# Optimization experiments

Hardware: AMD Instinct MI355X
Metric: run time of the kernel (lower is better)

Reference implementation:

```python
import jax, jax.numpy as jnp
import numpy as np

N = 20000      # nodes
E = 320000     # edges
IN = 128       # in_channels
HID = 64       # hidden_channels (per-head out dim, concat=False -> mean over heads)
HEADS = 4
NEG_SLOPE = 0.2


def setup_inputs() -> dict:
    key = jax.random.key(0)
    ks = jax.random.split(key, 18)
    g = lambda i, shape: jax.random.normal(ks[i], shape, dtype=jnp.float32) * 0.05
    return {
        "x": jax.random.normal(ks[0], (N, IN), dtype=jnp.float32),
        "edge_index": jax.random.randint(ks[1], (2, E), 0, N),
        # GATConv params: lin weight (no bias in PyG lin), att_src/att_dst, out bias
        "W0": g(2, (IN, HEADS * HID)),
        "W1": g(3, (HID, HEADS * HID)),
        "W2": g(4, (HID, HEADS * HID)),
        "W3": g(5, (HID, HEADS * HID)),
        "a_src": g(6, (4, HEADS, HID)),
        "a_dst": g(7, (4, HEADS, HID)),
        "gat_b": g(8, (4, HID)),
        # residual projection for layer 0 (in_channels != hidden_channels)
        "res_W": g(9, (IN, HID)),
        "res_b": g(10, (HID,)),
        # edge classifier MLP: 2*HID -> HID -> HID -> 1
        "lin_W0": g(11, (2 * HID, HID)),
        "lin_b0": g(12, (HID,)),
        "lin_W1": g(13, (HID, HID)),
        "lin_b1": g(14, (HID,)),
        "lin_W2": g(15, (HID, 1)),
        "lin_b2": g(16, (1,)),
    }


def gat_conv(x, src, dst, W, asrc, adst, b, n):
    # x: [n, F_in]; src/dst: [E_tot] (self-loops included); W: [F_in, H*C]
    h = (x @ W).reshape(n, HEADS, HID)                     # [n, H, C]
    s_src = (h * asrc).sum(-1)                             # [n, H]
    s_dst = (h * adst).sum(-1)                             # [n, H]
    e = jax.nn.leaky_relu(s_src[src] + s_dst[dst], NEG_SLOPE)  # [E_tot, H]
    # segment softmax over incoming edges of each dst node
    m = jax.ops.segment_max(e, dst, num_segments=n)        # [n, H]
    p = jnp.exp(e - m[dst])
    z = jax.ops.segment_sum(p, dst, num_segments=n)
    alpha = p / z[dst]                                     # [E_tot, H]
    out = jax.ops.segment_sum(alpha[:, :, None] * h[src], dst, num_segments=n)  # [n, H, C]
    return out.mean(axis=1) + b                            # concat=False -> mean over heads


def reference(x, edge_index, W0, W1, W2, W3, a_src, a_dst, gat_b,
              res_W, res_b, lin_W0, lin_b0, lin_W1, lin_b1, lin_W2, lin_b2):
    n = x.shape[0]
    loop = jnp.arange(n)
    src = jnp.concatenate([edge_index[0], loop])  # PyG GATConv adds self-loops
    dst = jnp.concatenate([edge_index[1], loop])
    Ws = [W0, W1, W2, W3]
    h = x
    for i in range(4):
        h_prev = h
        h = gat_conv(h, src, dst, Ws[i], a_src[i], a_dst[i], gat_b[i], n)
        if i == 0:
            h = h + h_prev @ res_W + res_b   # projected residual
        else:
            h = h + h_prev
        h = jax.nn.elu(h)
    row, col = edge_index[0], edge_index[1]
    er = jnp.concatenate([h[row], h[col]], axis=1)        # [E, 2*HID]
    er = jax.nn.relu(er @ lin_W0 + lin_b0)                # shapes differ -> no residual
    er = jax.nn.relu(er @ lin_W1 + lin_b1 + er)           # shapes match -> residual
    logits = er @ lin_W2 + lin_b2                          # [E, 1]
    return logits
```

## Files before the change

kernel.cpp:

```cpp
#include <hip/hip_runtime.h>
#include <hip/hip_bf16.h>

#define NSLOPE 0.2f

typedef short bf16x8 __attribute__((ext_vector_type(8)));
typedef float f32x4 __attribute__((ext_vector_type(4)));

__device__ __forceinline__ unsigned short f2b(float f) {
    unsigned u = __float_as_uint(f);
    unsigned r = (u + 0x7FFFu + ((u >> 16) & 1u)) >> 16;
    return (unsigned short)r;
}
__device__ __forceinline__ float b2f_lo(unsigned w) {
    return __uint_as_float(w << 16);
}
__device__ __forceinline__ float b2f_hi(unsigned w) {
    return __uint_as_float(w & 0xFFFF0000u);
}
__device__ __forceinline__ float b2f_s(short s) {
    return __uint_as_float(((unsigned)(unsigned short)s) << 16);
}
__device__ __forceinline__ unsigned packb(float lo, float hi) {
    return ((unsigned)f2b(hi) << 16) | (unsigned)f2b(lo);
}


__global__ __launch_bounds__(256) void hist_deg(const int* __restrict__ ei,
                                                int* __restrict__ deg, int E,
                                                int n) {
    int t = blockIdx.x * 256 + threadIdx.x;
    int Etot = E + n;
    if (t >= Etot) return;
    int d = (t < E) ? ei[E + t] : (t - E);
    atomicAdd(&deg[d], 1);
}

__global__ __launch_bounds__(256) void scan_blk(const int* __restrict__ deg,
                                                int* __restrict__ local,
                                                int* __restrict__ bsum, int n) {
    __shared__ int sm[256];
    const int base = blockIdx.x * 1024;
    const int t = threadIdx.x;
    const int i0 = base + t * 4;
    int v0 = 0, v1 = 0, v2 = 0, v3 = 0;
    if (i0 + 3 < n) {
        int4 v = *(const int4*)(deg + i0);
        v0 = v.x; v1 = v.y; v2 = v.z; v3 = v.w;
    } else {
        if (i0 < n) v0 = deg[i0];
        if (i0 + 1 < n) v1 = deg[i0 + 1];
        if (i0 + 2 < n) v2 = deg[i0 + 2];
    }
    int s = v0 + v1 + v2 + v3;
    sm[t] = s;
    __syncthreads();
    for (int off = 1; off < 256; off <<= 1) {
        int val = (t >= off) ? sm[t - off] : 0;
        __syncthreads();
        sm[t] += val;
        __syncthreads();
    }
    int ex = sm[t] - s;
    if (t == 255) bsum[blockIdx.x] = sm[255];
    if (i0 < n) local[i0] = ex;
    if (i0 + 1 < n) local[i0 + 1] = ex + v0;
    if (i0 + 2 < n) local[i0 + 2] = ex + v0 + v1;
    if (i0 + 3 < n) local[i0 + 3] = ex + v0 + v1 + v2;
}

__global__ __launch_bounds__(256) void scan_top(const int* __restrict__ bsum,
                                                int* __restrict__ boff,
                                                int nb) {
    __shared__ int sm[256];
    const int t = threadIdx.x;
    int s = (t < nb) ? bsum[t] : 0;
    sm[t] = s;
    __syncthreads();
    for (int off = 1; off < 256; off <<= 1) {
        int val = (t >= off) ? sm[t - off] : 0;
        __syncthreads();
        sm[t] += val;
        __syncthreads();
    }
    if (t < nb) boff[t] = sm[t] - s;
}

__global__ __launch_bounds__(256) void scan_add(const int* __restrict__ local,
                                                const int* __restrict__ boff,
                                                int* __restrict__ rowstart,
                                                int* __restrict__ cursor,
                                                int n, int Etot) {
    int i = blockIdx.x * 256 + threadIdx.x;
    if (i > n) return;
    if (i == n) {
        rowstart[n] = Etot;
        return;
    }
    int v = local[i] + boff[i >> 10];
    rowstart[i] = v;
    cursor[i] = v;
}

__global__ __launch_bounds__(256) void fill_csr(const int* __restrict__ ei,
                                                int* __restrict__ cursor,
                                                int2* __restrict__ csr2, int E,
                                                int n) {
    int t = blockIdx.x * 256 + threadIdx.x;
    int Etot = E + n;
    if (t >= Etot) return;
    int s, d;
    if (t < E) { s = ei[t]; d = ei[E + t]; } else { s = d = t - E; }
    int pos = atomicAdd(&cursor[d], 1);
    csr2[pos] = make_int2(s, d);
}

__global__ __launch_bounds__(256) void prep_weights(
    const float* __restrict__ W0, const float* __restrict__ W1,
    const float* __restrict__ W2, const float* __restrict__ W3,
    const float* __restrict__ resW, const float* __restrict__ linW0,
    const float* __restrict__ linW1, const float* __restrict__ linB0,
    short* __restrict__ WtC0, short* __restrict__ WtC1,
    short* __restrict__ WtC2, short* __restrict__ WtC3,
    short* __restrict__ WtR, short* __restrict__ WtU, short* __restrict__ WtV,
    short* __restrict__ WbT, float* __restrict__ bias128) {
    const int bx = blockIdx.x;
    if (bx < 4) {
        const float* src = (bx == 0) ? W0 : (bx == 1) ? W1 : (bx == 2) ? W2 : W3;
        short* dst = (bx == 0) ? WtC0 : (bx == 1) ? WtC1 : (bx == 2) ? WtC2 : WtC3;
        const int K = (bx == 0) ? 128 : 64;
        const int total = 64 * 4 * K;
        for (int idx = blockIdx.y * 256 + threadIdx.x; idx < total;
             idx += 256 * 16) {
            int j = idx / (4 * K);
            int rem = idx - j * 4 * K;
            int h = rem / K, k = rem - h * K;
            dst[idx] = (short)f2b(src[k * 256 + h * 64 + j]);
        }
        return;
    }
    const float* src;
    short* dst;
    int K, NC, rowoff = 0;
    switch (bx) {
        case 4: src = resW; dst = WtR; K = 128; NC = 64; break;
        case 5: src = linW0; dst = WtU; K = 64; NC = 64; break;
        case 6: src = linW0; dst = WtV; K = 64; NC = 64; rowoff = 64; break;
        case 7: src = linW1; dst = WbT; K = 64; NC = 64; break;
        default: {
            if (blockIdx.y == 0 && threadIdx.x < 128)
                bias128[threadIdx.x] =
                    (threadIdx.x < 64) ? linB0[threadIdx.x] : 0.f;
            return;
        }
    }
    for (int idx = blockIdx.y * 256 + threadIdx.x; idx < K * NC;
         idx += 256 * 16) {
        int k = idx / NC, nn = idx - k * NC;
        dst[nn * K + k] = (short)f2b(src[(k + rowoff) * NC + nn]);
    }
}

__global__ __launch_bounds__(256) void prep_wsd(
    const float* __restrict__ W0, const float* __restrict__ W1,
    const float* __restrict__ W2, const float* __restrict__ W3,
    const float* __restrict__ a_src, const float* __restrict__ a_dst,
    float* __restrict__ wsd0, float* __restrict__ wsdL) {
    const int l = blockIdx.x;
    const float* W = (l == 0) ? W0 : (l == 1) ? W1 : (l == 2) ? W2 : W3;
    const int K = (l == 0) ? 128 : 64;
    float* dst = (l == 0) ? wsd0 : wsdL + (l - 1) * 64 * 8;
    for (int idx = threadIdx.x; idx < K * 8; idx += 256) {
        int k = idx >> 3, j = idx & 7, h = j & 3;
        const float* av = ((j < 4) ? a_src : a_dst) + l * 256 + h * 64;
        const float* wr = W + k * 256 + h * 64;
        float s = 0.f;
#pragma unroll 8
        for (int c = 0; c < 64; ++c) s += wr[c] * av[c];
        dst[k * 8 + j] = s;
    }
}

__global__ __launch_bounds__(256) void convert_x_scores(
    const float* __restrict__ x, const float* __restrict__ wsd0,
    unsigned* __restrict__ xb2, float* __restrict__ Ssrc,
    float* __restrict__ Sdst, int n) {
    const int wid = threadIdx.x >> 6;
    const int lane = threadIdx.x & 63;
    const int node = blockIdx.x * 4 + wid;
    if (node >= n) return;
    float2 xv = *(const float2*)&x[(size_t)node * 128 + lane * 2];
    xb2[(size_t)node * 64 + lane] = packb(xv.x, xv.y);
    float pv[8];
    const float* w0 = &wsd0[(lane * 2) * 8];
    const float* w1 = &wsd0[(lane * 2 + 1) * 8];
#pragma unroll
    for (int j = 0; j < 8; ++j) pv[j] = xv.x * w0[j] + xv.y * w1[j];
#pragma unroll
    for (int off = 1; off < 64; off <<= 1) {
#pragma unroll
        for (int j = 0; j < 8; ++j) pv[j] += __shfl_xor(pv[j], off, 64);
    }
    if (lane == 0) {
        *(float4*)&Ssrc[node * 4] = make_float4(pv[0], pv[1], pv[2], pv[3]);
        *(float4*)&Sdst[node * 4] = make_float4(pv[4], pv[5], pv[6], pv[7]);
    }
}

template <int K, int NG, int OM>
__global__ __launch_bounds__(256) void mfma_gemm(
    const short* __restrict__ Xb, const short* __restrict__ Wt,
    const float* __restrict__ bias, float* __restrict__ OutF,
    short* __restrict__ OutB, int n) {
    constexpr int XSTR = K + 8;
    constexpr int NC = NG * 16;
    __shared__ __align__(16) short Xs[64 * XSTR];
    __shared__ __align__(16) short Ws[NC * 40];
    const int tid = threadIdx.x;
    const int nb = blockIdx.x * 64;
    constexpr int CH = K / 8;
    for (int idx = tid; idx < 64 * CH; idx += 256) {
        int row = idx / CH, c = idx - row * CH;
        uint4 v = make_uint4(0, 0, 0, 0);
        if (nb + row < n)
            v = *(const uint4*)(Xb + (size_t)(nb + row) * K + c * 8);
        *(uint4*)(Xs + row * XSTR + c * 8) = v;
    }
    const int wid = tid >> 6;
    const int lane = tid & 63;
    const int t = lane & 15, quad = lane >> 4;
    f32x4 acc[NG];
#pragma unroll
    for (int g = 0; g < NG; ++g) acc[g] = (f32x4){0.f, 0.f, 0.f, 0.f};
#pragma unroll 1
    for (int kc = 0; kc < K / 32; ++kc) {
        __syncthreads();
        for (int idx = tid; idx < NC * 4; idx += 256) {
            int row = idx >> 2, c = idx & 3;
            uint4 v = *(const uint4*)(Wt + (size_t)row * K + kc * 32 + c * 8);
            *(uint4*)(Ws + row * 40 + c * 8) = v;
        }
        __syncthreads();
        bf16x8 a =
            *(const bf16x8*)(Xs + (wid * 16 + t) * XSTR + kc * 32 + quad * 8);
#pragma unroll
        for (int g = 0; g < NG; ++g) {
            bf16x8 b = *(const bf16x8*)(Ws + (g * 16 + t) * 40 + quad * 8);
            acc[g] = __builtin_amdgcn_mfma_f32_16x16x32_bf16(a, b, acc[g], 0, 0, 0);
        }
    }
    float bv[NG];
#pragma unroll
    for (int g = 0; g < NG; ++g) bv[g] = bias ? bias[g * 16 + t] : 0.f;
#pragma unroll
    for (int r = 0; r < 4; ++r) {
        int node = nb + wid * 16 + quad * 4 + r;
        if (node >= n) continue;
        if (OM == 0) {
#pragma unroll
            for (int g = 0; g < NG; ++g)
                OutF[(size_t)node * NC + g * 16 + t] = acc[g][r] + bv[g];
        } else {
#pragma unroll
            for (int g = 0; g < NG; ++g)
                OutB[(size_t)node * NC + g * 16 + t] =
                    (short)f2b(acc[g][r] + bv[g]);
        }
    }
}

template <int KK, bool SCORES>
__global__ __launch_bounds__(256) void gemm_layer(
    const short* __restrict__ Xb, const short* __restrict__ Wt,
    const float* __restrict__ gbias, const float* __restrict__ resid,
    const float* __restrict__ wsd, float* __restrict__ feat,
    short* __restrict__ featb, float* __restrict__ Ssrc,
    float* __restrict__ Sdst, int n) {
    __shared__ __align__(16) short Xs[64 * 136];
    __shared__ __align__(16) short Ws[64 * 40];
    const int tid = threadIdx.x;
    const int nb = blockIdx.x * 64;
    const int wid = tid >> 6;
    const int lane = tid & 63;
    const int t = lane & 15, quad = lane >> 4;
    f32x4 acc[4];
#pragma unroll
    for (int g = 0; g < 4; ++g) acc[g] = (f32x4){0.f, 0.f, 0.f, 0.f};
#pragma unroll 1
    for (int c0 = 0; c0 < KK / 128; ++c0) {
        __syncthreads();
        for (int idx = tid; idx < 1024; idx += 256) {
            int row = idx >> 4, c = idx & 15;
            uint4 v = make_uint4(0, 0, 0, 0);
            if (nb + row < n)
                v = *(const uint4*)(Xb + (size_t)(nb + row) * KK + c0 * 128 +
                                    c * 8);
            *(uint4*)(Xs + row * 136 + c * 8) = v;
        }
#pragma unroll 1
        for (int kc = 0; kc < 4; ++kc) {
            __syncthreads();
            for (int idx = tid; idx < 256; idx += 256) {
                int row = idx >> 2, c = idx & 3;
                uint4 v = *(const uint4*)(Wt + (size_t)row * KK + c0 * 128 +
                                          kc * 32 + c * 8);
                *(uint4*)(Ws + row * 40 + c * 8) = v;
            }
            __syncthreads();
            bf16x8 a =
                *(const bf16x8*)(Xs + (wid * 16 + t) * 136 + kc * 32 + quad * 8);
#pragma unroll
            for (int g = 0; g < 4; ++g) {
                bf16x8 b = *(const bf16x8*)(Ws + (g * 16 + t) * 40 + quad * 8);
                acc[g] =
                    __builtin_amdgcn_mfma_f32_16x16x32_bf16(a, b, acc[g], 0, 0, 0);
            }
        }
    }
    float bv[4];
#pragma unroll
    for (int g = 0; g < 4; ++g) bv[g] = gbias[g * 16 + t];
    float wsv[4][8];
    if (SCORES) {
#pragma unroll
        for (int g = 0; g < 4; ++g) {
            float4 lo = *(const float4*)&wsd[(g * 16 + t) * 8];
            float4 hi = *(const float4*)&wsd[(g * 16 + t) * 8 + 4];
            wsv[g][0] = lo.x; wsv[g][1] = lo.y; wsv[g][2] = lo.z;
            wsv[g][3] = lo.w; wsv[g][4] = hi.x; wsv[g][5] = hi.y;
            wsv[g][6] = hi.z; wsv[g][7] = hi.w;
        }
    }
#pragma unroll
    for (int r = 0; r < 4; ++r) {
        int node = nb + wid * 16 + quad * 4 + r;
        bool ok = node < n;
        float val[4];
#pragma unroll
        for (int g = 0; g < 4; ++g) {
            float v = acc[g][r] + bv[g];
            if (ok) v += resid[(size_t)node * 64 + g * 16 + t];
            v = v > 0.f ? v : expm1f(v);
            val[g] = v;
            if (ok) {
                feat[(size_t)node * 64 + g * 16 + t] = v;
                featb[(size_t)node * 64 + g * 16 + t] = (short)f2b(v);
            }
        }
        if (SCORES) {
            float pv[8];
#pragma unroll
            for (int j = 0; j < 8; ++j) {
                pv[j] = val[0] * wsv[0][j] + val[1] * wsv[1][j] +
                        val[2] * wsv[2][j] + val[3] * wsv[3][j];
            }
#pragma unroll
            for (int off = 1; off < 16; off <<= 1) {
#pragma unroll
                for (int j = 0; j < 8; ++j) pv[j] += __shfl_xor(pv[j], off, 64);
            }
            if (t == 0 && ok) {
                *(float4*)&Ssrc[node * 4] =
                    make_float4(pv[0], pv[1], pv[2], pv[3]);
                *(float4*)&Sdst[node * 4] =
                    make_float4(pv[4], pv[5], pv[6], pv[7]);
            }
        }
    }
}

__global__ __launch_bounds__(256) void edge_scores(
    const int2* __restrict__ csr2, const float* __restrict__ Ssrc,
    const float* __restrict__ Sdst, float4* __restrict__ p4, int Etot) {
    int e = blockIdx.x * 256 + threadIdx.x;
    if (e >= Etot) return;
    int2 sd = csr2[e];
    float4 ss = *(const float4*)&Ssrc[sd.x * 4];
    float4 dd = *(const float4*)&Sdst[sd.y * 4];
    float c0 = ss.x + dd.x, c1 = ss.y + dd.y, c2 = ss.z + dd.z,
          c3 = ss.w + dd.w;
    c0 = c0 > 0.f ? c0 : NSLOPE * c0;
    c1 = c1 > 0.f ? c1 : NSLOPE * c1;
    c2 = c2 > 0.f ? c2 : NSLOPE * c2;
    c3 = c3 > 0.f ? c3 : NSLOPE * c3;
    p4[e] = make_float4(__expf(c0), __expf(c1), __expf(c2), __expf(c3));
}

__global__ __launch_bounds__(256) void gat_gather128(
    const int2* __restrict__ csr2, const int* __restrict__ rowstart,
    const float4* __restrict__ p4, const unsigned* __restrict__ xin,
    unsigned* __restrict__ aggB, int n) {
    const int wid = threadIdx.x >> 6;
    const int lane = threadIdx.x & 63;
    const int node = blockIdx.x * 4 + wid;
    if (node >= n) return;
    const int start = rowstart[node];
    const int end = rowstart[node + 1];
    float u00 = 0.f, u01 = 0.f, u10 = 0.f, u11 = 0.f;
    float u20 = 0.f, u21 = 0.f, u30 = 0.f, u31 = 0.f;
    float z0 = 0.f, z1 = 0.f, z2 = 0.f, z3 = 0.f;
#pragma unroll 4
    for (int e = start; e < end; ++e) {
        int sj = csr2[e].x;
        float4 p = p4[e];
        unsigned fv = xin[(size_t)sj * 64 + lane];
        float f0 = b2f_lo(fv), f1 = b2f_hi(fv);
        u00 += p.x * f0; u01 += p.x * f1;
        u10 += p.y * f0; u11 += p.y * f1;
        u20 += p.z * f0; u21 += p.z * f1;
        u30 += p.w * f0; u31 += p.w * f1;
        z0 += p.x; z1 += p.y; z2 += p.z; z3 += p.w;
    }
    float i0 = 0.25f / z0, i1 = 0.25f / z1, i2 = 0.25f / z2, i3 = 0.25f / z3;
    size_t base = (size_t)node * 256;
    aggB[base + lane] = packb(u00 * i0, u01 * i0);
    aggB[base + 64 + lane] = packb(u10 * i1, u11 * i1);
    aggB[base + 128 + lane] = packb(u20 * i2, u21 * i2);
    aggB[base + 192 + lane] = packb(u30 * i3, u31 * i3);
}

__global__ __launch_bounds__(256) void gat_gather64(
    const int2* __restrict__ csr2, const int* __restrict__ rowstart,
    const float4* __restrict__ p4, const unsigned* __restrict__ fin,
    unsigned* __restrict__ aggB, int n) {
    const int wid = threadIdx.x >> 6;
    const int lane = threadIdx.x & 63;
    const int half = lane >> 5;
    const int cl = lane & 31;
    const int node = blockIdx.x * 4 + wid;
    if (node >= n) return;
    const int start = rowstart[node];
    const int end = rowstart[node + 1];
    float u00 = 0.f, u01 = 0.f, u10 = 0.f, u11 = 0.f;
    float u20 = 0.f, u21 = 0.f, u30 = 0.f, u31 = 0.f;
    float z0 = 0.f, z1 = 0.f, z2 = 0.f, z3 = 0.f;
#pragma unroll 4
    for (int e = start + half; e < end; e += 2) {
        int sj = csr2[e].x;
        float4 p = p4[e];
        unsigned fv = fin[(size_t)sj * 32 + cl];
        float f0 = b2f_lo(fv), f1 = b2f_hi(fv);
        u00 += p.x * f0; u01 += p.x * f1;
        u10 += p.y * f0; u11 += p.y * f1;
        u20 += p.z * f0; u21 += p.z * f1;
        u30 += p.w * f0; u31 += p.w * f1;
        z0 += p.x; z1 += p.y; z2 += p.z; z3 += p.w;
    }
    u00 += __shfl_xor(u00, 32, 64); u01 += __shfl_xor(u01, 32, 64);
    u10 += __shfl_xor(u10, 32, 64); u11 += __shfl_xor(u11, 32, 64);
    u20 += __shfl_xor(u20, 32, 64); u21 += __shfl_xor(u21, 32, 64);
    u30 += __shfl_xor(u30, 32, 64); u31 += __shfl_xor(u31, 32, 64);
    z0 += __shfl_xor(z0, 32, 64); z1 += __shfl_xor(z1, 32, 64);
    z2 += __shfl_xor(z2, 32, 64); z3 += __shfl_xor(z3, 32, 64);
    if (half == 0) {
        float i0 = 0.25f / z0, i1 = 0.25f / z1, i2 = 0.25f / z2,
              i3 = 0.25f / z3;
        size_t base = (size_t)node * 128;
        aggB[base + cl] = packb(u00 * i0, u01 * i0);
        aggB[base + 32 + cl] = packb(u10 * i1, u11 * i1);
        aggB[base + 64 + cl] = packb(u20 * i2, u21 * i2);
        aggB[base + 96 + cl] = packb(u30 * i3, u31 * i3);
    }
}

__global__ __launch_bounds__(256) void edge_mlp3(
    const int* __restrict__ ei, const unsigned* __restrict__ UV,
    const short* __restrict__ WbT, const float* __restrict__ bb,
    const float* __restrict__ Wc, const float* __restrict__ bc,
    float* __restrict__ out, int E) {
    __shared__ __align__(16) short t1b[64 * 72];
    __shared__ __align__(16) short wbs[64 * 72];
    const int tid = threadIdx.x;
    const int eBase = blockIdx.x * 64;
    for (int idx = tid; idx < 512; idx += 256) {
        int row = idx >> 3, c = idx & 7;
        *(uint4*)(wbs + row * 72 + c * 8) =
            *(const uint4*)(WbT + row * 64 + c * 8);
    }
    {
        const int j = tid & 31;
        const int eg = tid >> 5;
        int rr[8], cc[8];
#pragma unroll
        for (int it = 0; it < 8; ++it) {
            int e = eBase + it * 8 + eg;
            rr[it] = (e < E) ? ei[e] : 0;
            cc[it] = (e < E) ? ei[E + e] : 0;
        }
#pragma unroll
        for (int it = 0; it < 8; ++it) {
            unsigned uu = UV[(size_t)rr[it] * 64 + j];
            unsigned vv = UV[(size_t)cc[it] * 64 + 32 + j];
            float lo = fmaxf(b2f_lo(uu) + b2f_lo(vv), 0.f);
            float hi = fmaxf(b2f_hi(uu) + b2f_hi(vv), 0.f);
            *(unsigned*)(t1b + (it * 8 + eg) * 72 + j * 2) = packb(lo, hi);
        }
    }
    __syncthreads();
    const int w = tid >> 6, lane = tid & 63;
    const int t = lane & 15, quad = lane >> 4;
    f32x4 acc[4];
#pragma unroll
    for (int g = 0; g < 4; ++g) acc[g] = (f32x4){0.f, 0.f, 0.f, 0.f};
#pragma unroll
    for (int kc = 0; kc < 2; ++kc) {
        bf16x8 a = *(const bf16x8*)(t1b + (w * 16 + t) * 72 + kc * 32 + quad * 8);
#pragma unroll
        for (int g = 0; g < 4; ++g) {
            bf16x8 b = *(const bf16x8*)(wbs + (g * 16 + t) * 72 + kc * 32 + quad * 8);
            acc[g] = __builtin_amdgcn_mfma_f32_16x16x32_bf16(a, b, acc[g], 0, 0, 0);
        }
    }
    float wcv[4], bbv[4];
#pragma unroll
    for (int g = 0; g < 4; ++g) {
        wcv[g] = Wc[g * 16 + t];
        bbv[g] = bb[g * 16 + t];
    }
    const float bcv = bc[0];
#pragma unroll
    for (int r = 0; r < 4; ++r) {
        int el = w * 16 + quad * 4 + r;
        float part = 0.f;
#pragma unroll
        for (int g = 0; g < 4; ++g) {
            float t1v = b2f_s(t1b[el * 72 + g * 16 + t]);
            float t2 = fmaxf(acc[g][r] + bbv[g] + t1v, 0.f);
            part += t2 * wcv[g];
        }
        part += __shfl_xor(part, 1, 64);
        part += __shfl_xor(part, 2, 64);
        part += __shfl_xor(part, 4, 64);
        part += __shfl_xor(part, 8, 64);
        int e = eBase + el;
        if (t == 0 && e < E) out[e] = part + bcv;
    }
}

extern "C" void kernel_launch(void* const* d_in, const int* in_sizes, int n_in,
                              void* d_out, int out_size, void* d_ws,
                              size_t ws_size, hipStream_t stream) {
    const float* x = (const float*)d_in[0];
    const int* ei = (const int*)d_in[1];
    const float* W0 = (const float*)d_in[2];
    const float* W1 = (const float*)d_in[3];
    const float* W2 = (const float*)d_in[4];
    const float* W3 = (const float*)d_in[5];
    const float* a_src = (const float*)d_in[6];
    const float* a_dst = (const float*)d_in[7];
    const float* gat_b = (const float*)d_in[8];
    const float* res_W = (const float*)d_in[9];
    const float* res_b = (const float*)d_in[10];
    const float* lin_W0 = (const float*)d_in[11];
    const float* lin_b0 = (const float*)d_in[12];
    const float* lin_W1 = (const float*)d_in[13];
    const float* lin_b1 = (const float*)d_in[14];
    const float* lin_W2 = (const float*)d_in[15];
    const float* lin_b2 = (const float*)d_in[16];
    float* out = (float*)d_out;

    const int N = in_sizes[0] / 128;
    const int E = in_sizes[1] / 2;
    const int Etot = E + N;

    char* ws = (char*)d_ws;
    unsigned* aggB = (unsigned*)ws;
    float* featA = (float*)(aggB + (size_t)N * 256);
    float* featB = featA + (size_t)N * 64;
    short* featbA = (short*)(featB + (size_t)N * 64);
    short* featbB = featbA + (size_t)N * 64;
    float* res = (float*)(featbB + (size_t)N * 64);
    short* xb = (short*)(res + (size_t)N * 64);
    float* Ssrc = (float*)(xb + (size_t)N * 128);
    float* Sdst = Ssrc + (size_t)N * 4;
    short* WtC0 = (short*)(Sdst + (size_t)N * 4);
    short* WtC1 = WtC0 + 64 * 512;
    short* WtC2 = WtC1 + 64 * 256;
    short* WtC3 = WtC2 + 64 * 256;
    short* WtR = WtC3 + 64 * 256;
    short* WtU = WtR + 64 * 128;
    short* WtV = WtU + 64 * 64;
    short* WbT = WtV + 64 * 64;
    float* wsd0 = (float*)(WbT + 64 * 64);
    float* wsdL = wsd0 + 128 * 8;
    float* bias128 = wsdL + 3 * 64 * 8;
    int* deg = (int*)(bias128 + 128);
    int* rowstart = deg + N;
    int* cursor = rowstart + N + 1;
    int* locals = cursor + N;
    int* bsum = locals + N;
    int* boff = bsum + 256;
    int2* csr2 = (int2*)(((size_t)(boff + 256) + 15) & ~(size_t)15);
    float4* p4 = (float4*)(((size_t)(csr2 + Etot) + 15) & ~(size_t)15);
    unsigned* UVb = aggB;

    const int gemmBlocks = (N + 63) / 64;
    const int edgeBlocks = (Etot + 255) / 256;
    const int nodeW = (N + 3) / 4;
    const int scanBlocks = (N + 1023) / 1024;

    hipMemsetAsync(deg, 0, (size_t)N * sizeof(int), stream);
    hist_deg<<<edgeBlocks, 256, 0, stream>>>(ei, deg, E, N);
    scan_blk<<<scanBlocks, 256, 0, stream>>>(deg, locals, bsum, N);
    scan_top<<<1, 256, 0, stream>>>(bsum, boff, scanBlocks);
    scan_add<<<(N + 256) / 256, 256, 0, stream>>>(locals, boff, rowstart,
                                                  cursor, N, Etot);
    fill_csr<<<edgeBlocks, 256, 0, stream>>>(ei, cursor, csr2, E, N);

    prep_weights<<<dim3(9, 16), 256, 0, stream>>>(
        W0, W1, W2, W3, res_W, lin_W0, lin_W1, lin_b0, WtC0, WtC1, WtC2, WtC3,
        WtR, WtU, WtV, WbT, bias128);
    prep_wsd<<<4, 256, 0, stream>>>(W0, W1, W2, W3, a_src, a_dst, wsd0, wsdL);
    convert_x_scores<<<nodeW, 256, 0, stream>>>(x, wsd0, (unsigned*)xb, Ssrc,
                                                Sdst, N);
    mfma_gemm<128, 4, 0><<<gemmBlocks, 256, 0, stream>>>(xb, WtR, res_b, res,
                                                         nullptr, N);

    edge_scores<<<edgeBlocks, 256, 0, stream>>>(csr2, Ssrc, Sdst, p4, Etot);
    gat_gather128<<<nodeW, 256, 0, stream>>>(csr2, rowstart, p4,
                                             (const unsigned*)xb, aggB, N);
    gemm_layer<512, true><<<gemmBlocks, 256, 0, stream>>>(
        (const short*)aggB, WtC0, gat_b, res, wsdL, featA, featbA, Ssrc, Sdst,
        N);
    const short* WtCs[3] = {WtC1, WtC2, WtC3};
    float* feats[4] = {featA, featB, featA, featB};
    short* featbs[4] = {featbA, featbB, featbA, featbB};
    for (int i = 1; i < 4; ++i) {
        edge_scores<<<edgeBlocks, 256, 0, stream>>>(csr2, Ssrc, Sdst, p4, Etot);
        gat_gather64<<<nodeW, 256, 0, stream>>>(
            csr2, rowstart, p4, (const unsigned*)featbs[i - 1], aggB, N);
        if (i < 3)
            gemm_layer<256, true><<<gemmBlocks, 256, 0, stream>>>(
                (const short*)aggB, WtCs[i - 1], gat_b + i * 64, feats[i - 1],
                wsdL + i * 64 * 8, feats[i], featbs[i], Ssrc, Sdst, N);
        else
            gemm_layer<256, false><<<gemmBlocks, 256, 0, stream>>>(
                (const short*)aggB, WtCs[i - 1], gat_b + i * 64, feats[i - 1],
                nullptr, feats[i], featbs[i], Ssrc, Sdst, N);
    }

    mfma_gemm<64, 8, 2><<<gemmBlocks, 256, 0, stream>>>(
        featbB, WtU, bias128, nullptr, (short*)UVb, N);
    edge_mlp3<<<(E + 63) / 64, 256, 0, stream>>>(ei, UVb, WbT, lin_b1, lin_W2,
                                                 lin_b2, out, E);
}
```

Before: 353.7 us.

## Fuse edge score computation into gather kernels and shrink CSR to source-only indices

```diff
diff --git a/kernel.cpp b/kernel.cpp
--- a/kernel.cpp
+++ b/kernel.cpp
@@ -103,7 +103,7 @@
 
 __global__ __launch_bounds__(256) void fill_csr(const int* __restrict__ ei,
                                                 int* __restrict__ cursor,
-                                                int2* __restrict__ csr2, int E,
+                                                int* __restrict__ csrS, int E,
                                                 int n) {
     int t = blockIdx.x * 256 + threadIdx.x;
     int Etot = E + n;
@@ -111,7 +111,7 @@
     int s, d;
     if (t < E) { s = ei[t]; d = ei[E + t]; } else { s = d = t - E; }
     int pos = atomicAdd(&cursor[d], 1);
-    csr2[pos] = make_int2(s, d);
+    csrS[pos] = s;
 }
 
 __global__ __launch_bounds__(256) void prep_weights(
@@ -368,49 +368,61 @@
     }
 }
 
-__global__ __launch_bounds__(256) void edge_scores(
-    const int2* __restrict__ csr2, const float* __restrict__ Ssrc,
-    const float* __restrict__ Sdst, float4* __restrict__ p4, int Etot) {
-    int e = blockIdx.x * 256 + threadIdx.x;
-    if (e >= Etot) return;
-    int2 sd = csr2[e];
-    float4 ss = *(const float4*)&Ssrc[sd.x * 4];
-    float4 dd = *(const float4*)&Sdst[sd.y * 4];
-    float c0 = ss.x + dd.x, c1 = ss.y + dd.y, c2 = ss.z + dd.z,
-          c3 = ss.w + dd.w;
-    c0 = c0 > 0.f ? c0 : NSLOPE * c0;
-    c1 = c1 > 0.f ? c1 : NSLOPE * c1;
-    c2 = c2 > 0.f ? c2 : NSLOPE * c2;
-    c3 = c3 > 0.f ? c3 : NSLOPE * c3;
-    p4[e] = make_float4(__expf(c0), __expf(c1), __expf(c2), __expf(c3));
-}
-
 __global__ __launch_bounds__(256) void gat_gather128(
-    const int2* __restrict__ csr2, const int* __restrict__ rowstart,
-    const float4* __restrict__ p4, const unsigned* __restrict__ xin,
-    unsigned* __restrict__ aggB, int n) {
+    const int* __restrict__ csrS, const int* __restrict__ rowstart,
+    const float* __restrict__ Ssrc, const float* __restrict__ Sdst,
+    const unsigned* __restrict__ xin, unsigned* __restrict__ aggB, int n) {
     const int wid = threadIdx.x >> 6;
     const int lane = threadIdx.x & 63;
     const int node = blockIdx.x * 4 + wid;
     if (node >= n) return;
     const int start = rowstart[node];
     const int end = rowstart[node + 1];
+    const float4 sd = *(const float4*)&Sdst[node * 4];
     float u00 = 0.f, u01 = 0.f, u10 = 0.f, u11 = 0.f;
     float u20 = 0.f, u21 = 0.f, u30 = 0.f, u31 = 0.f;
-    float z0 = 0.f, z1 = 0.f, z2 = 0.f, z3 = 0.f;
+    float zp0 = 0.f, zp1 = 0.f, zp2 = 0.f, zp3 = 0.f;
+    for (int base = start; base < end; base += 64) {
+        const int cnt = min(64, end - base);
+        int sreg = 0;
+        float p0r = 0.f, p1r = 0.f, p2r = 0.f, p3r = 0.f;
+        if (lane < cnt) {
+            sreg = csrS[base + lane];
+            float4 ss = *(const float4*)&Ssrc[sreg * 4];
+            float c0 = ss.x + sd.x, c1 = ss.y + sd.y;
+            float c2 = ss.z + sd.z, c3 = ss.w + sd.w;
+            c0 = c0 > 0.f ? c0 : NSLOPE * c0;
+            c1 = c1 > 0.f ? c1 : NSLOPE * c1;
+            c2 = c2 > 0.f ? c2 : NSLOPE * c2;
+            c3 = c3 > 0.f ? c3 : NSLOPE * c3;
+            p0r = __expf(c0); p1r = __expf(c1);
+            p2r = __expf(c2); p3r = __expf(c3);
+            zp0 += p0r; zp1 += p1r; zp2 += p2r; zp3 += p3r;
+        }
 #pragma unroll 4
-    for (int e = start; e < end; ++e) {
-        int sj = csr2[e].x;
-        float4 p = p4[e];
-        unsigned fv = xin[(size_t)sj * 64 + lane];
-        float f0 = b2f_lo(fv), f1 = b2f_hi(fv);
-        u00 += p.x * f0; u01 += p.x * f1;
-        u10 += p.y * f0; u11 += p.y * f1;
-        u20 += p.z * f0; u21 += p.z * f1;
-        u30 += p.w * f0; u31 += p.w * f1;
-        z0 += p.x; z1 += p.y; z2 += p.z; z3 += p.w;
-    }
-    float i0 = 0.25f / z0, i1 = 0.25f / z1, i2 = 0.25f / z2, i3 = 0.25f / z3;
+        for (int j = 0; j < cnt; ++j) {
+            int sj = __shfl(sreg, j, 64);
+            float p0 = __shfl(p0r, j, 64);
+            float p1 = __shfl(p1r, j, 64);
+            float p2 = __shfl(p2r, j, 64);
+            float p3 = __shfl(p3r, j, 64);
+            unsigned fv = xin[(size_t)sj * 64 + lane];
+            float f0 = b2f_lo(fv), f1 = b2f_hi(fv);
+            u00 += p0 * f0; u01 += p0 * f1;
+            u10 += p1 * f0; u11 += p1 * f1;
+            u20 += p2 * f0; u21 += p2 * f1;
+            u30 += p3 * f0; u31 += p3 * f1;
+        }
+    }
+#pragma unroll
+    for (int off = 1; off < 64; off <<= 1) {
+        zp0 += __shfl_xor(zp0, off, 64);
+        zp1 += __shfl_xor(zp1, off, 64);
+        zp2 += __shfl_xor(zp2, off, 64);
+        zp3 += __shfl_xor(zp3, off, 64);
+    }
+    float i0 = 0.25f / zp0, i1 = 0.25f / zp1;
+    float i2 = 0.25f / zp2, i3 = 0.25f / zp3;
     size_t base = (size_t)node * 256;
     aggB[base + lane] = packb(u00 * i0, u01 * i0);
     aggB[base + 64 + lane] = packb(u10 * i1, u11 * i1);
@@ -419,9 +431,9 @@
 }
 
 __global__ __launch_bounds__(256) void gat_gather64(
-    const int2* __restrict__ csr2, const int* __restrict__ rowstart,
-    const float4* __restrict__ p4, const unsigned* __restrict__ fin,
-    unsigned* __restrict__ aggB, int n) {
+    const int* __restrict__ csrS, const int* __restrict__ rowstart,
+    const float* __restrict__ Ssrc, const float* __restrict__ Sdst,
+    const unsigned* __restrict__ fin, unsigned* __restrict__ aggB, int n) {
     const int wid = threadIdx.x >> 6;
     const int lane = threadIdx.x & 63;
     const int half = lane >> 5;
@@ -430,30 +442,59 @@
     if (node >= n) return;
     const int start = rowstart[node];
     const int end = rowstart[node + 1];
+    const float4 sd = *(const float4*)&Sdst[node * 4];
     float u00 = 0.f, u01 = 0.f, u10 = 0.f, u11 = 0.f;
     float u20 = 0.f, u21 = 0.f, u30 = 0.f, u31 = 0.f;
-    float z0 = 0.f, z1 = 0.f, z2 = 0.f, z3 = 0.f;
+    float zp0 = 0.f, zp1 = 0.f, zp2 = 0.f, zp3 = 0.f;
+    for (int base = start; base < end; base += 64) {
+        const int cnt = min(64, end - base);
+        int sreg = 0;
+        float p0r = 0.f, p1r = 0.f, p2r = 0.f, p3r = 0.f;
+        if (lane < cnt) {
+            sreg = csrS[base + lane];
+            float4 ss = *(const float4*)&Ssrc[sreg * 4];
+            float c0 = ss.x + sd.x, c1 = ss.y + sd.y;
+            float c2 = ss.z + sd.z, c3 = ss.w + sd.w;
+            c0 = c0 > 0.f ? c0 : NSLOPE * c0;
+            c1 = c1 > 0.f ? c1 : NSLOPE * c1;
+            c2 = c2 > 0.f ? c2 : NSLOPE * c2;
+            c3 = c3 > 0.f ? c3 : NSLOPE * c3;
+            p0r = __expf(c0); p1r = __expf(c1);
+            p2r = __expf(c2); p3r = __expf(c3);
+            zp0 += p0r; zp1 += p1r; zp2 += p2r; zp3 += p3r;
+        }
 #pragma unroll 4
-    for (int e = start + half; e < end; e += 2) {
-        int sj = csr2[e].x;
-        float4 p = p4[e];
-        unsigned fv = fin[(size_t)sj * 32 + cl];
-        float f0 = b2f_lo(fv), f1 = b2f_hi(fv);
-        u00 += p.x * f0; u01 += p.x * f1;
-        u10 += p.y * f0; u11 += p.y * f1;
-        u20 += p.z * f0; u21 += p.z * f1;
-        u30 += p.w * f0; u31 += p.w * f1;
-        z0 += p.x; z1 += p.y; z2 += p.z; z3 += p.w;
+        for (int j = 0; j < cnt; j += 2) {
+            int idx = j + half;
+            int sj = __shfl(sreg, idx, 64);
+            float p0 = __shfl(p0r, idx, 64);
+            float p1 = __shfl(p1r, idx, 64);
+            float p2 = __shfl(p2r, idx, 64);
+            float p3 = __shfl(p3r, idx, 64);
+            if (idx < cnt) {
+                unsigned fv = fin[(size_t)sj * 32 + cl];
+                float f0 = b2f_lo(fv), f1 = b2f_hi(fv);
+                u00 += p0 * f0; u01 += p0 * f1;
+                u10 += p1 * f0; u11 += p1 * f1;
+                u20 += p2 * f0; u21 += p2 * f1;
+                u30 += p3 * f0; u31 += p3 * f1;
+            }
+        }
     }
     u00 += __shfl_xor(u00, 32, 64); u01 += __shfl_xor(u01, 32, 64);
     u10 += __shfl_xor(u10, 32, 64); u11 += __shfl_xor(u11, 32, 64);
     u20 += __shfl_xor(u20, 32, 64); u21 += __shfl_xor(u21, 32, 64);
     u30 += __shfl_xor(u30, 32, 64); u31 += __shfl_xor(u31, 32, 64);
-    z0 += __shfl_xor(z0, 32, 64); z1 += __shfl_xor(z1, 32, 64);
-    z2 += __shfl_xor(z2, 32, 64); z3 += __shfl_xor(z3, 32, 64);
+#pragma unroll
+    for (int off = 1; off < 64; off <<= 1) {
+        zp0 += __shfl_xor(zp0, off, 64);
+        zp1 += __shfl_xor(zp1, off, 64);
+        zp2 += __shfl_xor(zp2, off, 64);
+        zp3 += __shfl_xor(zp3, off, 64);
+    }
     if (half == 0) {
-        float i0 = 0.25f / z0, i1 = 0.25f / z1, i2 = 0.25f / z2,
-              i3 = 0.25f / z3;
+        float i0 = 0.25f / zp0, i1 = 0.25f / zp1;
+        float i2 = 0.25f / zp2, i3 = 0.25f / zp3;
         size_t base = (size_t)node * 128;
         aggB[base + cl] = packb(u00 * i0, u01 * i0);
         aggB[base + 32 + cl] = packb(u10 * i1, u11 * i1);
@@ -589,8 +630,7 @@
     int* locals = cursor + N;
     int* bsum = locals + N;
     int* boff = bsum + 256;
-    int2* csr2 = (int2*)(((size_t)(boff + 256) + 15) & ~(size_t)15);
-    float4* p4 = (float4*)(((size_t)(csr2 + Etot) + 15) & ~(size_t)15);
+    int* csrS = boff + 256;
     unsigned* UVb = aggB;
 
     const int gemmBlocks = (N + 63) / 64;
@@ -604,7 +644,7 @@
     scan_top<<<1, 256, 0, stream>>>(bsum, boff, scanBlocks);
     scan_add<<<(N + 256) / 256, 256, 0, stream>>>(locals, boff, rowstart,
                                                   cursor, N, Etot);
-    fill_csr<<<edgeBlocks, 256, 0, stream>>>(ei, cursor, csr2, E, N);
+    fill_csr<<<edgeBlocks, 256, 0, stream>>>(ei, cursor, csrS, E, N);
 
     prep_weights<<<dim3(9, 16), 256, 0, stream>>>(
         W0, W1, W2, W3, res_W, lin_W0, lin_W1, lin_b0, WtC0, WtC1, WtC2, WtC3,
@@ -615,8 +655,7 @@
     mfma_gemm<128, 4, 0><<<gemmBlocks, 256, 0, stream>>>(xb, WtR, res_b, res,
                                                          nullptr, N);
 
-    edge_scores<<<edgeBlocks, 256, 0, stream>>>(csr2, Ssrc, Sdst, p4, Etot);
-    gat_gather128<<<nodeW, 256, 0, stream>>>(csr2, rowstart, p4,
+    gat_gather128<<<nodeW, 256, 0, stream>>>(csrS, rowstart, Ssrc, Sdst,
                                              (const unsigned*)xb, aggB, N);
     gemm_layer<512, true><<<gemmBlocks, 256, 0, stream>>>(
         (const short*)aggB, WtC0, gat_b, res, wsdL, featA, featbA, Ssrc, Sdst,
@@ -625,9 +664,9 @@
     float* feats[4] = {featA, featB, featA, featB};
     short* featbs[4] = {featbA, featbB, featbA, featbB};
     for (int i = 1; i < 4; ++i) {
-        edge_scores<<<edgeBlocks, 256, 0, stream>>>(csr2, Ssrc, Sdst, p4, Etot);
         gat_gather64<<<nodeW, 256, 0, stream>>>(
-            csr2, rowstart, p4, (const unsigned*)featbs[i - 1], aggB, N);
+            csrS, rowstart, Ssrc, Sdst, (const unsigned*)featbs[i - 1], aggB,
+            N);
         if (i < 3)
             gemm_layer<256, true><<<gemmBlocks, 256, 0, stream>>>(
                 (const short*)aggB, WtCs[i - 1], gat_b + i * 64, feats[i - 1],
```

Result: slower. 364.2 us (+3.0%).
